# Kernel tuning notes

Measured on AMD Instinct MI355X. Metric: run time of the kernel, lower is better.

Reference implementation:

```python
import jax, jax.numpy as jnp
import numpy as np

H = 128  # hidden_size

def _band_agg(h):
    # Equivalent to bmm(adj, h) with adj = degree-normalized tridiagonal
    # (self + left + right neighbor), degree=3 interior, 2 at endpoints,
    # normalization adj/(deg+1e-8) as in the torch module.
    B, S, D = h.shape
    hp = jnp.pad(h, ((0, 0), (1, 1), (0, 0)))
    s = hp[:, :-2] + hp[:, 1:-1] + hp[:, 2:]            # [B,S,D] neighbor sum
    deg = jnp.full((S,), 3.0, dtype=h.dtype).at[0].set(2.0).at[S - 1].set(2.0)
    return s / (deg + 1e-8)[None, :, None]


def setup_inputs() -> dict:
    key = jax.random.key(0)
    ks = jax.random.split(key, 16)
    f32 = jnp.float32
    p = lambda k, shp: (jax.random.normal(k, shp, dtype=f32) * 0.05)
    return {
        "x": jax.random.normal(ks[0], (32, 2048, 6), dtype=f32),
        "enc_w1": p(ks[1], (6, H)),   "enc_b1": p(ks[2], (H,)),
        "enc_w2": p(ks[3], (H, H)),   "enc_b2": p(ks[4], (H,)),
        "gc1_w": p(ks[5], (H, H)),    "gc1_b": p(ks[6], (H,)),
        "gc2_w": p(ks[7], (H, H)),    "gc2_b": p(ks[8], (H,)),
        "gc3_w": p(ks[9], (H, H)),    "gc3_b": p(ks[10], (H,)),
        "cls_w1": p(ks[11], (H, H // 2)), "cls_b1": p(ks[12], (H // 2,)),
        "cls_w2": p(ks[13], (H // 2, 3)), "cls_b2": p(ks[14], (3,)),
    }


def reference(x, enc_w1, enc_b1, enc_w2, enc_b2,
              gc1_w, gc1_b, gc2_w, gc2_b, gc3_w, gc3_b,
              cls_w1, cls_b1, cls_w2, cls_b2):
    # node encoder: Linear -> ReLU -> Linear
    h = jax.nn.relu(x @ enc_w1 + enc_b1) @ enc_w2 + enc_b2
    # three graph convolutions: linear, normalized tridiagonal aggregate, relu
    h = jax.nn.relu(_band_agg(h @ gc1_w + gc1_b))
    h = jax.nn.relu(_band_agg(h @ gc2_w + gc2_b))
    h = jax.nn.relu(_band_agg(h @ gc3_w + gc3_b))
    # AdaptiveAvgPool1d(1) over seq dim after transpose == mean over nodes
    pooled = h.mean(axis=1)                              # [B, H]
    # classifier (dropout inactive in eval)
    return jax.nn.relu(pooled @ cls_w1 + cls_b1) @ cls_w2 + cls_b2
```

## Files before the change

### kernel.cpp

```cpp
#include <hip/hip_runtime.h>

#define SEQ  2048
#define HID  128
#define NB   32
#define TILE 58
#define GX   36
#define MSTR 67

typedef float f2    __attribute__((ext_vector_type(2)));
typedef float f32x4 __attribute__((ext_vector_type(4)));
typedef short bf16x8 __attribute__((ext_vector_type(8)));

__device__ __forceinline__ void split_bf16(float v, short& h, short& l) {
  unsigned u = __float_as_uint(v);
  unsigned r = (u + 0x7fffu + ((u >> 16) & 1u)) >> 16;
  h = (short)r;
  const float hf = __uint_as_float(r << 16);
  const float lo = v - hf;
  unsigned u2 = __float_as_uint(lo);
  unsigned r2 = (u2 + 0x7fffu + ((u2 >> 16) & 1u)) >> 16;
  l = (short)r2;
}

__global__ __launch_bounds__(256) void prep_kernel(
    const float* __restrict__ enc_w2, const float* __restrict__ enc_b2,
    const float* __restrict__ gc1_w, const float* __restrict__ gc1_b,
    const float* __restrict__ gc2_w, const float* __restrict__ gc3_w,
    short* __restrict__ Wf, float* __restrict__ bp, unsigned* __restrict__ cnt)
{
  const int tid = threadIdx.x;
  const int bid = blockIdx.x;

  if (bid == 96) {
    if (tid < 128) {
      float s = gc1_b[tid];
      for (int k = 0; k < 128; ++k) s = fmaf(enc_b2[k], gc1_w[k * 128 + tid], s);
      bp[tid] = s;
    }
    if (tid < NB) cnt[tid] = 0u;
    return;
  }

  const int L = bid >> 5, bx = bid & 31;
  short* hi = Wf + L * 32768;
  short* lo = hi + 16384;

  if (L == 0) {
    __shared__ float As[32 * 128];
    __shared__ float Bs[128 * 16];
    const int k0 = (bx >> 3) * 32, n0 = (bx & 7) * 16;
    for (int i = tid; i < 1024; i += 256)
      ((f32x4*)As)[i] = ((const f32x4*)(enc_w2 + k0 * 128))[i];
    for (int i = tid; i < 512; i += 256) {
      const int t = i >> 2, q = i & 3;
      ((f32x4*)Bs)[i] = *(const f32x4*)(gc1_w + t * 128 + n0 + q * 4);
    }
    __syncthreads();
    #pragma unroll
    for (int e = 0; e < 2; ++e) {
      const int f = tid + e * 256;
      const int l = f >> 3, j = f & 7;
      const float* ar = As + ((l >> 4) * 8 + j) * 128;
      const int nn = l & 15;
      float s0 = 0.f, s1 = 0.f, s2 = 0.f, s3 = 0.f;
      for (int t = 0; t < 128; t += 4) {
        s0 = fmaf(ar[t + 0], Bs[(t + 0) * 16 + nn], s0);
        s1 = fmaf(ar[t + 1], Bs[(t + 1) * 16 + nn], s1);
        s2 = fmaf(ar[t + 2], Bs[(t + 2) * 16 + nn], s2);
        s3 = fmaf(ar[t + 3], Bs[(t + 3) * 16 + nn], s3);
      }
      short h, lw;
      split_bf16((s0 + s1) + (s2 + s3), h, lw);
      hi[bx * 512 + f] = h; lo[bx * 512 + f] = lw;
    }
  } else {
    const float* __restrict__ SW = (L == 1) ? gc2_w : gc3_w;
    const int ks = bx >> 3, nt = bx & 7;
    for (int f = tid; f < 512; f += 256) {
      const int l = f >> 3, j = f & 7;
      const int k = ks * 32 + (l >> 4) * 8 + j;
      const int n = nt * 16 + (l & 15);
      short h, lw;
      split_bf16(SW[k * 128 + n], h, lw);
      hi[bx * 512 + f] = h; lo[bx * 512 + f] = lw;
    }
  }
}

__global__ __launch_bounds__(256) void fused_kernel(
    const float* __restrict__ x,
    const float* __restrict__ enc_w1, const float* __restrict__ enc_b1,
    const short* __restrict__ Wf, const float* __restrict__ bp,
    const float* __restrict__ gc2_b, const float* __restrict__ gc3_b,
    float* __restrict__ partial, unsigned* __restrict__ cnt,
    const float* __restrict__ cls_w1, const float* __restrict__ cls_b1,
    const float* __restrict__ cls_w2, const float* __restrict__ cls_b2,
    float* __restrict__ out)
{
  __shared__ float hT[HID * MSTR];
  __shared__ float wsmall[7 * HID];
  __shared__ float psum[256];
  __shared__ int lastf;

  const int tid  = threadIdx.x;
  const int lane = tid & 63;
  const int w    = tid >> 6;
  const int gxb  = blockIdx.x, b = blockIdx.y;
  const int s0   = gxb * TILE;

  for (int f = tid; f < 7 * HID; f += 256)
    wsmall[f] = (f < 6 * HID) ? enc_w1[f] : enc_b1[f - 6 * HID];

  const int sm = s0 - 3 + lane;
  float xv[6];
  if (sm >= 0 && sm < SEQ) {
    const f2* xp = (const f2*)(x + ((long long)b * SEQ + sm) * 6);
    const f2 a0 = xp[0], a1 = xp[1], a2 = xp[2];
    xv[0] = a0.x; xv[1] = a0.y; xv[2] = a1.x;
    xv[3] = a1.y; xv[4] = a2.x; xv[5] = a2.y;
  } else {
    #pragma unroll
    for (int k = 0; k < 6; ++k) xv[k] = 0.f;
  }
  __syncthreads();
  {
    const int c0 = w * 32;
    float4 a4[8];
    #pragma unroll
    for (int q = 0; q < 8; ++q) a4[q] = make_float4(0.f, 0.f, 0.f, 0.f);
    #pragma unroll
    for (int k = 0; k < 6; ++k) {
      #pragma unroll
      for (int q = 0; q < 8; ++q) {
        const float4 wv = *(const float4*)&wsmall[k * HID + c0 + q * 4];
        a4[q].x = fmaf(xv[k], wv.x, a4[q].x);
        a4[q].y = fmaf(xv[k], wv.y, a4[q].y);
        a4[q].z = fmaf(xv[k], wv.z, a4[q].z);
        a4[q].w = fmaf(xv[k], wv.w, a4[q].w);
      }
    }
    #pragma unroll
    for (int q = 0; q < 8; ++q) {
      const float4 bb = *(const float4*)&wsmall[6 * HID + c0 + q * 4];
      const int c = c0 + q * 4;
      hT[(c + 0) * MSTR + lane] = fmaxf(a4[q].x + bb.x, 0.f);
      hT[(c + 1) * MSTR + lane] = fmaxf(a4[q].y + bb.y, 0.f);
      hT[(c + 2) * MSTR + lane] = fmaxf(a4[q].z + bb.z, 0.f);
      hT[(c + 3) * MSTR + lane] = fmaxf(a4[q].w + bb.w, 0.f);
    }
  }
  __syncthreads();

  const int mt   = w * 16 + (lane & 15);
  const int koct = (lane >> 4) * 8;
  const int stt  = s0 - 3 + mt;
  const float invdA = (stt == 0 || stt == SEQ - 1) ? (1.0f / (2.0f + 1e-8f))
                                                   : (1.0f / (3.0f + 1e-8f));
  const int mm = (mt == 0) ? 0 : mt - 1;
  const int mp = (mt == 63) ? 63 : mt + 1;

  #pragma unroll 1
  for (int L = 0; L < 3; ++L) {
    const short* WfL = Wf + L * 32768;
    const bf16x8* Bhi = (const bf16x8*)WfL;
    const bf16x8* Blo = (const bf16x8*)(WfL + 16384);
    const float* bias = (L == 0) ? bp : (L == 1) ? gc2_b : gc3_b;

    f32x4 acc_[8];
    #pragma unroll
    for (int nt = 0; nt < 8; ++nt) acc_[nt] = (f32x4){0.f, 0.f, 0.f, 0.f};

    #pragma unroll 1
    for (int ks = 0; ks < 4; ++ks) {
      const int fb = ks * 512 + lane;
      bf16x8 bh[8], bl[8];
      #pragma unroll
      for (int nt = 0; nt < 8; ++nt) {
        bh[nt] = Bhi[fb + nt * 64];
        bl[nt] = Blo[fb + nt * 64];
      }
      bf16x8 ah, al;
      const float* pa = &hT[(ks * 32 + koct) * MSTR];
      #pragma unroll
      for (int j = 0; j < 8; ++j) {
        float v;
        if (L == 0) {
          v = pa[j * MSTR + mt];
        } else {
          v = (pa[j * MSTR + mm] + pa[j * MSTR + mt] + pa[j * MSTR + mp]) * invdA;
          v = fmaxf(v, 0.f);
        }
        short h, lo;
        split_bf16(v, h, lo);
        ah[j] = h; al[j] = lo;
      }
      #pragma unroll
      for (int nt = 0; nt < 8; ++nt) {
        acc_[nt] = __builtin_amdgcn_mfma_f32_16x16x32_bf16(ah, bh[nt], acc_[nt], 0, 0, 0);
        acc_[nt] = __builtin_amdgcn_mfma_f32_16x16x32_bf16(ah, bl[nt], acc_[nt], 0, 0, 0);
        acc_[nt] = __builtin_amdgcn_mfma_f32_16x16x32_bf16(al, bh[nt], acc_[nt], 0, 0, 0);
      }
    }
    __syncthreads();

    {
      const int n0 = lane & 15;
      const int mrow0 = w * 16 + (lane >> 4) * 4;
      #pragma unroll
      for (int nt = 0; nt < 8; ++nt) {
        const float bn = bias[nt * 16 + n0];
        float* pw = &hT[(nt * 16 + n0) * MSTR];
        #pragma unroll
        for (int r = 0; r < 4; ++r) {
          const int m = mrow0 + r;
          const int s = s0 - 3 + m;
          const bool vld = (s >= 0 && s < SEQ);
          pw[m] = vld ? (acc_[nt][r] + bn) : 0.f;
        }
      }
    }
    __syncthreads();
  }

  {
    const int c = tid & 127, half = tid >> 7;
    float ps = 0.f;
    const float* pc = &hT[c * MSTR];
    #pragma unroll 1
    for (int r = 0; r < 29; ++r) {
      const int m = 3 + half * 29 + r;
      const int s = s0 + half * 29 + r;
      if (s < SEQ) {
        const float invd = (s == 0 || s == SEQ - 1) ? (1.0f / (2.0f + 1e-8f))
                                                    : (1.0f / (3.0f + 1e-8f));
        ps += fmaxf((pc[m - 1] + pc[m] + pc[m + 1]) * invd, 0.f);
      }
    }
    psum[tid] = ps;
  }
  __syncthreads();

  if (tid < 128) {
    __hip_atomic_store(&partial[((long long)b * GX + gxb) * HID + tid],
                       psum[tid] + psum[tid + 128],
                       __ATOMIC_RELAXED, __HIP_MEMORY_SCOPE_AGENT);
  }
  asm volatile("s_waitcnt vmcnt(0)" ::: "memory");
  __syncthreads();
  if (tid == 0) {
    const unsigned old = __hip_atomic_fetch_add(&cnt[b], 1u, __ATOMIC_ACQ_REL,
                                                __HIP_MEMORY_SCOPE_AGENT);
    lastf = (old == GX - 1) ? 1 : 0;
  }
  __syncthreads();
  if (!lastf) return;

  if (tid < 128) {
    float a = 0.f;
    #pragma unroll
    for (int g = 0; g < GX; ++g)
      a += __hip_atomic_load(&partial[((long long)b * GX + g) * HID + tid],
                             __ATOMIC_RELAXED, __HIP_MEMORY_SCOPE_AGENT);
    psum[tid] = a * (1.0f / 2048.0f);
  }
  __syncthreads();
  if (tid < 64) {
    float h = cls_b1[tid];
    for (int k = 0; k < 128; ++k) h = fmaf(psum[k], cls_w1[k * 64 + tid], h);
    psum[128 + tid] = fmaxf(h, 0.f);
  }
  __syncthreads();
  if (tid < 3) {
    float o = cls_b2[tid];
    for (int k = 0; k < 64; ++k) o = fmaf(psum[128 + k], cls_w2[k * 3 + tid], o);
    out[b * 3 + tid] = o;
  }
}

extern "C" void kernel_launch(void* const* d_in, const int* in_sizes, int n_in,
                              void* d_out, int out_size, void* d_ws, size_t ws_size,
                              hipStream_t stream) {
  (void)in_sizes; (void)n_in; (void)out_size; (void)ws_size;
  const float* x      = (const float*)d_in[0];
  const float* enc_w1 = (const float*)d_in[1];
  const float* enc_b1 = (const float*)d_in[2];
  const float* enc_w2 = (const float*)d_in[3];
  const float* enc_b2 = (const float*)d_in[4];
  const float* gc1_w  = (const float*)d_in[5];
  const float* gc1_b  = (const float*)d_in[6];
  const float* gc2_w  = (const float*)d_in[7];
  const float* gc2_b  = (const float*)d_in[8];
  const float* gc3_w  = (const float*)d_in[9];
  const float* gc3_b  = (const float*)d_in[10];
  const float* cls_w1 = (const float*)d_in[11];
  const float* cls_b1 = (const float*)d_in[12];
  const float* cls_w2 = (const float*)d_in[13];
  const float* cls_b2 = (const float*)d_in[14];

  float* bpv     = (float*)d_ws;
  short* Wfrag   = (short*)(bpv + 128);
  float* partial = (float*)(Wfrag + 3 * 2 * 16384);
  unsigned* cntb = (unsigned*)(partial + (long long)NB * GX * HID);

  prep_kernel<<<dim3(97), 256, 0, stream>>>(enc_w2, enc_b2, gc1_w, gc1_b,
                                            gc2_w, gc3_w, Wfrag, bpv, cntb);
  fused_kernel<<<dim3(GX, NB), 256, 0, stream>>>(
      x, enc_w1, enc_b1, Wfrag, bpv, gc2_b, gc3_b, partial, cntb,
      cls_w1, cls_b1, cls_w2, cls_b2, (float*)d_out);
}
```

Measured before the change: 145.2 us.

## Double-buffer weight fragments in registers and use packed hardware bf16 conversion

The three-layer loop is fully unrolled into explicit k-steps. While the current step runs its MFMAs, the next step's hi/lo weight fragments are loaded from global memory into a second register buffer. The first fragment load is issued before the encoder runs, so global-load latency overlaps with compute, including across layer boundaries. The software bf16 hi/lo split is replaced with v_cvt_pk_bf16_f32 packed conversions, and the completion counter atomic is relaxed from acq_rel to relaxed. This costs many more VGPRs for the duplicate buffers, which may cut occupancy, and the relaxed counter weakens the ordering guarantee that the last block's reads of partial sums depend on.

```diff
diff --git a/kernel.cpp b/kernel.cpp
--- a/kernel.cpp
+++ b/kernel.cpp
@@ -10,6 +10,7 @@
 typedef float f2    __attribute__((ext_vector_type(2)));
 typedef float f32x4 __attribute__((ext_vector_type(4)));
 typedef short bf16x8 __attribute__((ext_vector_type(8)));
+typedef unsigned u32x4 __attribute__((ext_vector_type(4)));
 
 __device__ __forceinline__ void split_bf16(float v, short& h, short& l) {
   unsigned u = __float_as_uint(v);
@@ -20,6 +21,12 @@
   unsigned u2 = __float_as_uint(lo);
   unsigned r2 = (u2 + 0x7fffu + ((u2 >> 16) & 1u)) >> 16;
   l = (short)r2;
+}
+
+__device__ __forceinline__ unsigned cvt_pk_bf16(float a, float b) {
+  unsigned r;
+  asm("v_cvt_pk_bf16_f32 %0, %1, %2" : "=v"(r) : "v"(a), "v"(b));
+  return r;
 }
 
 __global__ __launch_bounds__(256) void prep_kernel(
@@ -87,6 +94,73 @@
   }
 }
 
+
+#define LOADB(BH, BL, LC, KS)                                                  \
+  {                                                                            \
+    _Pragma("unroll")                                                          \
+    for (int nt = 0; nt < 8; ++nt) {                                           \
+      BH[nt] = Bf[(LC) * 4096 + (KS) * 512 + nt * 64 + lane];                  \
+      BL[nt] = Bf[(LC) * 4096 + 2048 + (KS) * 512 + nt * 64 + lane];           \
+    }                                                                          \
+  }
+
+#define KSTEP(LC, KS, BH_CUR, BL_CUR, BH_NXT, BL_NXT, LN, KN, DO_PREF)         \
+  {                                                                            \
+    if (DO_PREF) LOADB(BH_NXT, BL_NXT, LN, KN);                                \
+    bf16x8 ah, al;                                                             \
+    {                                                                          \
+      const float* pa = &hT[((KS) * 32 + koct) * MSTR];                        \
+      float v[8];                                                              \
+      _Pragma("unroll")                                                        \
+      for (int j = 0; j < 8; ++j) {                                            \
+        if ((LC) == 0) {                                                       \
+          v[j] = pa[j * MSTR + mt];                                            \
+        } else {                                                               \
+          const float t = (pa[j * MSTR + mm] + pa[j * MSTR + mt] +             \
+                           pa[j * MSTR + mp]) * invdA;                         \
+          v[j] = fmaxf(t, 0.f);                                                \
+        }                                                                      \
+      }                                                                        \
+      u32x4 hv, lv;                                                            \
+      _Pragma("unroll")                                                        \
+      for (int q = 0; q < 4; ++q) {                                            \
+        const unsigned hp = cvt_pk_bf16(v[2 * q], v[2 * q + 1]);               \
+        const float h0 = __uint_as_float(hp << 16);                            \
+        const float h1 = __uint_as_float(hp & 0xffff0000u);                    \
+        hv[q] = hp;                                                            \
+        lv[q] = cvt_pk_bf16(v[2 * q] - h0, v[2 * q + 1] - h1);                 \
+      }                                                                        \
+      ah = __builtin_bit_cast(bf16x8, hv);                                     \
+      al = __builtin_bit_cast(bf16x8, lv);                                     \
+    }                                                                          \
+    _Pragma("unroll")                                                          \
+    for (int nt = 0; nt < 8; ++nt) {                                           \
+      acc_[nt] = __builtin_amdgcn_mfma_f32_16x16x32_bf16(ah, BH_CUR[nt], acc_[nt], 0, 0, 0); \
+      acc_[nt] = __builtin_amdgcn_mfma_f32_16x16x32_bf16(ah, BL_CUR[nt], acc_[nt], 0, 0, 0); \
+      acc_[nt] = __builtin_amdgcn_mfma_f32_16x16x32_bf16(al, BH_CUR[nt], acc_[nt], 0, 0, 0); \
+    }                                                                          \
+  }
+
+#define EPILOGUE(BIAS)                                                         \
+  {                                                                            \
+    __syncthreads();                                                           \
+    const int n0 = lane & 15;                                                  \
+    const int mrow0 = w * 16 + (lane >> 4) * 4;                                \
+    _Pragma("unroll")                                                          \
+    for (int nt = 0; nt < 8; ++nt) {                                           \
+      const float bn = (BIAS)[nt * 16 + n0];                                   \
+      float* pw = &hT[(nt * 16 + n0) * MSTR];                                  \
+      _Pragma("unroll")                                                        \
+      for (int r = 0; r < 4; ++r) {                                            \
+        const int m = mrow0 + r;                                               \
+        const int s = s0 - 3 + m;                                              \
+        const bool vld = (s >= 0 && s < SEQ);                                  \
+        pw[m] = vld ? (acc_[nt][r] + bn) : 0.f;                                \
+      }                                                                        \
+    }                                                                          \
+    __syncthreads();                                                           \
+  }
+
 __global__ __launch_bounds__(256) void fused_kernel(
     const float* __restrict__ x,
     const float* __restrict__ enc_w1, const float* __restrict__ enc_b1,
@@ -107,6 +181,7 @@
   const int w    = tid >> 6;
   const int gxb  = blockIdx.x, b = blockIdx.y;
   const int s0   = gxb * TILE;
+  const bf16x8* Bf = (const bf16x8*)Wf;
 
   for (int f = tid; f < 7 * HID; f += 256)
     wsmall[f] = (f < 6 * HID) ? enc_w1[f] : enc_b1[f - 6 * HID];
@@ -123,6 +198,10 @@
     for (int k = 0; k < 6; ++k) xv[k] = 0.f;
   }
   __syncthreads();
+
+  bf16x8 bhA[8], blA[8], bhB[8], blB[8];
+  LOADB(bhA, blA, 0, 0);
+
   {
     const int c0 = w * 32;
     float4 a4[8];
@@ -159,67 +238,35 @@
   const int mm = (mt == 0) ? 0 : mt - 1;
   const int mp = (mt == 63) ? 63 : mt + 1;
 
-  #pragma unroll 1
-  for (int L = 0; L < 3; ++L) {
-    const short* WfL = Wf + L * 32768;
-    const bf16x8* Bhi = (const bf16x8*)WfL;
-    const bf16x8* Blo = (const bf16x8*)(WfL + 16384);
-    const float* bias = (L == 0) ? bp : (L == 1) ? gc2_b : gc3_b;
-
+  {
     f32x4 acc_[8];
     #pragma unroll
     for (int nt = 0; nt < 8; ++nt) acc_[nt] = (f32x4){0.f, 0.f, 0.f, 0.f};
-
-    #pragma unroll 1
-    for (int ks = 0; ks < 4; ++ks) {
-      const int fb = ks * 512 + lane;
-      bf16x8 bh[8], bl[8];
-      #pragma unroll
-      for (int nt = 0; nt < 8; ++nt) {
-        bh[nt] = Bhi[fb + nt * 64];
-        bl[nt] = Blo[fb + nt * 64];
-      }
-      bf16x8 ah, al;
-      const float* pa = &hT[(ks * 32 + koct) * MSTR];
-      #pragma unroll
-      for (int j = 0; j < 8; ++j) {
-        float v;
-        if (L == 0) {
-          v = pa[j * MSTR + mt];
-        } else {
-          v = (pa[j * MSTR + mm] + pa[j * MSTR + mt] + pa[j * MSTR + mp]) * invdA;
-          v = fmaxf(v, 0.f);
-        }
-        short h, lo;
-        split_bf16(v, h, lo);
-        ah[j] = h; al[j] = lo;
-      }
-      #pragma unroll
-      for (int nt = 0; nt < 8; ++nt) {
-        acc_[nt] = __builtin_amdgcn_mfma_f32_16x16x32_bf16(ah, bh[nt], acc_[nt], 0, 0, 0);
-        acc_[nt] = __builtin_amdgcn_mfma_f32_16x16x32_bf16(ah, bl[nt], acc_[nt], 0, 0, 0);
-        acc_[nt] = __builtin_amdgcn_mfma_f32_16x16x32_bf16(al, bh[nt], acc_[nt], 0, 0, 0);
-      }
-    }
-    __syncthreads();
-
-    {
-      const int n0 = lane & 15;
-      const int mrow0 = w * 16 + (lane >> 4) * 4;
-      #pragma unroll
-      for (int nt = 0; nt < 8; ++nt) {
-        const float bn = bias[nt * 16 + n0];
-        float* pw = &hT[(nt * 16 + n0) * MSTR];
-        #pragma unroll
-        for (int r = 0; r < 4; ++r) {
-          const int m = mrow0 + r;
-          const int s = s0 - 3 + m;
-          const bool vld = (s >= 0 && s < SEQ);
-          pw[m] = vld ? (acc_[nt][r] + bn) : 0.f;
-        }
-      }
-    }
-    __syncthreads();
+    KSTEP(0, 0, bhA, blA, bhB, blB, 0, 1, true)
+    KSTEP(0, 1, bhB, blB, bhA, blA, 0, 2, true)
+    KSTEP(0, 2, bhA, blA, bhB, blB, 0, 3, true)
+    KSTEP(0, 3, bhB, blB, bhA, blA, 1, 0, true)
+    EPILOGUE(bp)
+  }
+  {
+    f32x4 acc_[8];
+    #pragma unroll
+    for (int nt = 0; nt < 8; ++nt) acc_[nt] = (f32x4){0.f, 0.f, 0.f, 0.f};
+    KSTEP(1, 0, bhA, blA, bhB, blB, 1, 1, true)
+    KSTEP(1, 1, bhB, blB, bhA, blA, 1, 2, true)
+    KSTEP(1, 2, bhA, blA, bhB, blB, 1, 3, true)
+    KSTEP(1, 3, bhB, blB, bhA, blA, 2, 0, true)
+    EPILOGUE(gc2_b)
+  }
+  {
+    f32x4 acc_[8];
+    #pragma unroll
+    for (int nt = 0; nt < 8; ++nt) acc_[nt] = (f32x4){0.f, 0.f, 0.f, 0.f};
+    KSTEP(2, 0, bhA, blA, bhB, blB, 2, 1, true)
+    KSTEP(2, 1, bhB, blB, bhA, blA, 2, 2, true)
+    KSTEP(2, 2, bhA, blA, bhB, blB, 2, 3, true)
+    KSTEP(2, 3, bhB, blB, bhA, blA, 2, 0, false)
+    EPILOGUE(gc3_b)
   }
 
   {
@@ -248,7 +295,7 @@
   asm volatile("s_waitcnt vmcnt(0)" ::: "memory");
   __syncthreads();
   if (tid == 0) {
-    const unsigned old = __hip_atomic_fetch_add(&cnt[b], 1u, __ATOMIC_ACQ_REL,
+    const unsigned old = __hip_atomic_fetch_add(&cnt[b], 1u, __ATOMIC_RELAXED,
                                                 __HIP_MEMORY_SCOPE_AGENT);
     lastf = (old == GX - 1) ? 1 : 0;
   }
```

After: 148.6 us. 2.4% more time.
